# Kernel tuning notes

Measured on AMD Instinct MI355X. Metric: run time of the kernel, lower is better.

## Reference

```python
import jax, jax.numpy as jnp
import numpy as np

B, S, T = 32, 512, 128   # batch, source chars, target (protoform) chars
V, L = 128, 5            # char vocab len(C2I), number of languages
E, H, F = 512, 1024, 2048  # embedding_dim, model_size, feedforward_dim
START_CHAR, SEP_LANG = 1, L - 1


def setup_inputs() -> dict:
    key = jax.random.key(0)
    ks = jax.random.split(key, 32)
    f32 = jnp.float32

    def n(k, shape, fan_in):
        return jax.random.normal(k, shape, dtype=f32) * (1.0 / np.sqrt(fan_in))

    inp = {
        "src_chars": jax.random.randint(ks[0], (B, S), 0, V),
        "src_langs": jax.random.randint(ks[1], (B, S), 0, L),
        "tgt_chars": jax.random.randint(ks[2], (B, T), 0, V),
        # embedding feature extractor
        "char_emb": jax.random.normal(ks[3], (V, E), dtype=f32) * 0.02,
        "lang_emb": jax.random.normal(ks[4], (L, E), dtype=f32) * 0.02,
        "fc_W": n(ks[5], (E, 2 * E), 2 * E),
        "fc_b": jnp.zeros((E,), f32),
        # encoder GRU (PyTorch gate layout r,z,n)
        "enc_Wi": n(ks[6], (3 * H, E), E),
        "enc_Wh": n(ks[7], (3 * H, H), H),
        "enc_bi": jnp.zeros((3 * H,), f32),
        "enc_bh": jnp.zeros((3 * H,), f32),
        # decoder GRU, input = [E ; H]
        "dec_Wi": n(ks[8], (3 * H, E + H), E + H),
        "dec_Wh": n(ks[9], (3 * H, H), H),
        "dec_bi": jnp.zeros((3 * H,), f32),
        "dec_bh": jnp.zeros((3 * H,), f32),
        # attention
        "Wq": n(ks[10], (H, H), H),
        "Wk": n(ks[11], (H, H), H),
        "Wcs": n(ks[12], (H, E), E),
        # MLP H -> 2F -> F -> V
        "W1": n(ks[13], (2 * F, H), H),
        "b1": jnp.zeros((2 * F,), f32),
        "W2": n(ks[14], (F, 2 * F), 2 * F),
        "b2": jnp.zeros((F,), f32),
        "W3": n(ks[15], (V, F), F),
    }
    return inp


def _gru_step(h, x, Wi, Wh, bi, bh):
    gi = x @ Wi.T + bi            # [B, 3H]
    gh = h @ Wh.T + bh            # [B, 3H]
    ir, iz, inn = jnp.split(gi, 3, axis=-1)
    hr, hz, hn = jnp.split(gh, 3, axis=-1)
    r = jax.nn.sigmoid(ir + hr)
    z = jax.nn.sigmoid(iz + hz)
    n = jnp.tanh(inn + r * hn)
    return (1.0 - z) * n + z * h


def _mlp(x, W1, b1, W2, b2, W3):
    h = jax.nn.relu(x @ W1.T + b1)
    h = jax.nn.relu(h @ W2.T + b2)
    return h @ W3.T               # [B, V]


def reference(src_chars, src_langs, tgt_chars,
              char_emb, lang_emb, fc_W, fc_b,
              enc_Wi, enc_Wh, enc_bi, enc_bh,
              dec_Wi, dec_Wh, dec_bi, dec_bh,
              Wq, Wk, Wcs,
              W1, b1, W2, b2, W3):
    # --- feature extraction: concat(char_emb, lang_emb) -> Linear(2E -> E) ---
    def embed(c_idx, l_idx):
        ce = char_emb[c_idx]                       # [..., E]
        le = lang_emb[l_idx]                       # [..., E]
        return jnp.concatenate([ce, le], -1) @ fc_W.T + fc_b

    encoded = embed(src_chars, src_langs)          # [B, S, E]

    # --- encoder GRU over source chars ---
    def enc_step(h, x_t):
        h = _gru_step(h, x_t, enc_Wi, enc_Wh, enc_bi, enc_bh)
        return h, h

    h0 = jnp.zeros((encoded.shape[0], enc_Wh.shape[1]), encoded.dtype)
    _, enc_states = jax.lax.scan(enc_step, h0, jnp.swapaxes(encoded, 0, 1))
    enc_states = jnp.swapaxes(enc_states, 0, 1)    # [B, S, H]

    # precompute attention values: W_c_s(encoded) + W_key(keys)  [B, S, H]
    att_vals = encoded @ Wcs.T + enc_states @ Wk.T

    # --- initial decoder step: <s> embedding + last encoder state ---
    start_emb = embed(jnp.full((encoded.shape[0],), START_CHAR),
                      jnp.full((encoded.shape[0],), SEP_LANG))  # [B, E]
    context0 = enc_states[:, -1]                   # [B, H]
    d0 = jnp.zeros_like(context0)
    dec_h = _gru_step(d0, jnp.concatenate([start_emb, context0], -1),
                      dec_Wi, dec_Wh, dec_bi, dec_bh)

    tgt_emb = embed(tgt_chars, jnp.full_like(tgt_chars, SEP_LANG))  # [B, T, E]

    # --- decode T steps with teacher forcing ---
    def dec_step(carry, x_t):
        h, ctx = carry
        scores_t = _mlp(h + ctx, W1, b1, W2, b2, W3)           # [B, V]
        q = h @ Wq.T                                           # [B, H]
        att = jnp.einsum('bsh,bh->bs', enc_states, q)
        w = jax.nn.softmax(att, axis=-1)
        ctx_new = jnp.einsum('bs,bsh->bh', w, att_vals)        # [B, H]
        h_new = _gru_step(h, jnp.concatenate([x_t, ctx_new], -1),
                          dec_Wi, dec_Wh, dec_bi, dec_bh)
        return (h_new, ctx_new), scores_t

    (_, _), scores = jax.lax.scan(dec_step, (dec_h, context0),
                                  jnp.swapaxes(tgt_emb, 0, 1))
    return jnp.swapaxes(scores, 0, 1)              # [B, T, V]
```

## Files before the change

kernel.cpp:

```cpp
#include <hip/hip_runtime.h>
#include <math.h>


#define Bb 32
#define Ss 512
#define Tt 128
#define Vv 128
#define Hh 1024
#define H3 3072
#define APAD 40

typedef __attribute__((ext_vector_type(8))) short bf16x8;
typedef __attribute__((ext_vector_type(4))) float f32x4;

__device__ inline f32x4 mfma_bf16(bf16x8 a, bf16x8 b, f32x4 c) {
  return __builtin_amdgcn_mfma_f32_16x16x32_bf16(a, b, c, 0, 0, 0);
}
__device__ inline unsigned short f2bf(float f) {
  unsigned u = __builtin_bit_cast(unsigned, f);
  unsigned r = (u + 0x7fffu + ((u >> 16) & 1u)) >> 16;
  return (unsigned short)r;
}
__device__ inline float lof(unsigned u) { return __builtin_bit_cast(float, u << 16); }
__device__ inline float hif(unsigned u) { return __builtin_bit_cast(float, u & 0xffff0000u); }
__device__ inline float bf2f(unsigned short h) {
  return __builtin_bit_cast(float, ((unsigned)h) << 16);
}

#define O_ESBF   0UL
#define O_ESQ    33554432UL
#define O_AVBF   67108864UL
#define O_HCBF   100663296UL
#define O_WHE    109051904UL
#define O_WHD    115343360UL
#define O_WIC    121634816UL
#define O_WKB    127926272UL
#define O_WQT    130023424UL
#define O_W1B    132120576UL
#define O_W2B    140509184UL
#define O_W3B    157286400UL
#define O_XCAT   157810688UL
#define O_EMBFC  160432128UL
#define O_GITAB  161742848UL
#define O_AVTAB  169607168UL
#define O_DGIXT  172228608UL
#define O_GH     173801472UL
#define O_GI     174194688UL
#define O_H      174587904UL
#define O_HBF    174718976UL
#define O_CTX    174784512UL
#define O_CTXBF  174915584UL
#define O_ATTL   174981120UL

__global__ void k_xcat(const float* __restrict__ ce, const float* __restrict__ le,
                       float* __restrict__ xcat) {
  int row = blockIdx.x;
  int l = row >> 7, c = row & 127;
  int i = threadIdx.x * 4;
  float4 v;
  if (i < 512) v = *(const float4*)(ce + c * 512 + i);
  else         v = *(const float4*)(le + l * 512 + (i - 512));
  *(float4*)(xcat + (size_t)row * 1024 + i) = v;
}

__global__ void k_cltab(const int* __restrict__ sc, const int* __restrict__ sl,
                        int* __restrict__ cl) {
  int i = blockIdx.x * 256 + threadIdx.x;
  int b = i >> 9, s = i & 511;
  cl[s * 32 + b] = sl[b * Ss + s] * 128 + sc[b * Ss + s];
}

__global__ void k_cvt(const float* __restrict__ src, int ld, int lc,
                      unsigned short* __restrict__ dst) {
  size_t i = ((size_t)blockIdx.x * 256 + threadIdx.x) * 8;
  size_t r = i >> lc;
  int c = (int)(i & ((1u << lc) - 1));
  const float* s = src + r * (size_t)ld + c;
  float4 v0 = *(const float4*)s;
  float4 v1 = *(const float4*)(s + 4);
  union { unsigned short us[8]; uint4 u; } o;
  o.us[0] = f2bf(v0.x); o.us[1] = f2bf(v0.y); o.us[2] = f2bf(v0.z); o.us[3] = f2bf(v0.w);
  o.us[4] = f2bf(v1.x); o.us[5] = f2bf(v1.y); o.us[6] = f2bf(v1.z); o.us[7] = f2bf(v1.w);
  *(uint4*)(dst + i) = o.u;
}

__global__ void k_transcvt(const float* __restrict__ in, unsigned short* __restrict__ out) {
  __shared__ float t[32][33];
  int c0 = blockIdx.x * 32, r0 = blockIdx.y * 32;
  int tx = threadIdx.x, ty = threadIdx.y;
  for (int i = ty; i < 32; i += 8)
    t[i][tx] = in[(size_t)(r0 + i) * 1024 + c0 + tx];
  __syncthreads();
  for (int i = ty; i < 32; i += 8)
    out[(size_t)(c0 + i) * 1024 + r0 + tx] = f2bf(t[tx][i]);
}

template <bool BIAS>
__global__ __launch_bounds__(256) void k_gemm(
    const float* __restrict__ A, int lda, const float* __restrict__ W, int ldw,
    const float* __restrict__ bias, float* __restrict__ C, int ldc, int K) {
  __shared__ float As[8][128];
  __shared__ float Ws[8][128];
  int tid = threadIdx.x;
  int n0 = blockIdx.x * 128, m0 = blockIdx.y * 128;
  int tx = tid & 15, ty = tid >> 4;
  int lrow = tid >> 1, lseg = (tid & 1) * 4;
  const float* Ap = A + (size_t)(m0 + lrow) * lda + lseg;
  const float* Wp = W + (size_t)(n0 + lrow) * ldw + lseg;
  float acc[8][8];
#pragma unroll
  for (int i = 0; i < 8; ++i)
#pragma unroll
    for (int j = 0; j < 8; ++j) acc[i][j] = 0.f;
  for (int kt = 0; kt < K; kt += 8) {
    float4 av = *(const float4*)(Ap + kt);
    float4 wv = *(const float4*)(Wp + kt);
    __syncthreads();
    As[lseg + 0][lrow] = av.x; As[lseg + 1][lrow] = av.y;
    As[lseg + 2][lrow] = av.z; As[lseg + 3][lrow] = av.w;
    Ws[lseg + 0][lrow] = wv.x; Ws[lseg + 1][lrow] = wv.y;
    Ws[lseg + 2][lrow] = wv.z; Ws[lseg + 3][lrow] = wv.w;
    __syncthreads();
#pragma unroll
    for (int kk = 0; kk < 8; ++kk) {
      float a[8], b[8];
      *(float4*)(a + 0) = *(const float4*)(&As[kk][ty * 8 + 0]);
      *(float4*)(a + 4) = *(const float4*)(&As[kk][ty * 8 + 4]);
      *(float4*)(b + 0) = *(const float4*)(&Ws[kk][tx * 8 + 0]);
      *(float4*)(b + 4) = *(const float4*)(&Ws[kk][tx * 8 + 4]);
#pragma unroll
      for (int i = 0; i < 8; ++i)
#pragma unroll
        for (int j = 0; j < 8; ++j) acc[i][j] = fmaf(a[i], b[j], acc[i][j]);
    }
  }
#pragma unroll
  for (int i = 0; i < 8; ++i) {
    int r = m0 + ty * 8 + i;
#pragma unroll
    for (int j = 0; j < 8; ++j) {
      int c = n0 + tx * 8 + j;
      float v = acc[i][j];
      if (BIAS) v += bias[c];
      C[(size_t)r * ldc + c] = v;
    }
  }
}

template <int EPI, bool RELU, bool BIAS>
__global__ __launch_bounds__(256) void k_bgemm(
    const unsigned short* __restrict__ A, int lda,
    const unsigned short* __restrict__ W, int ldw,
    const float* __restrict__ bias, void* __restrict__ Cout, int ldc, int K,
    const float* __restrict__ avtab, const int* __restrict__ gl,
    const int* __restrict__ gc) {
  __shared__ unsigned short As[128 * APAD];
  __shared__ unsigned short Bs[128 * APAD];
  int tid = threadIdx.x;
  int n0 = blockIdx.x * 128, m0 = blockIdx.y * 128;
  int w = tid >> 6, l = tid & 63;
  int mw = (w & 1) * 64, nw = (w >> 1) * 64;
  int lrow = tid >> 1, lk = (tid & 1) * 16;
  const unsigned short* Ap = A + (size_t)(m0 + lrow) * lda + lk;
  const unsigned short* Wp = W + (size_t)(n0 + lrow) * ldw + lk;
  int fr = l & 15, fk = (l >> 4) * 8;
  f32x4 acc[4][4];
#pragma unroll
  for (int i = 0; i < 4; ++i)
#pragma unroll
    for (int j = 0; j < 4; ++j) acc[i][j] = (f32x4){0.f, 0.f, 0.f, 0.f};
  for (int kt = 0; kt < K; kt += 32) {
    uint4 a0 = *(const uint4*)(Ap + kt);
    uint4 a1 = *(const uint4*)(Ap + kt + 8);
    uint4 b0 = *(const uint4*)(Wp + kt);
    uint4 b1 = *(const uint4*)(Wp + kt + 8);
    __syncthreads();
    *(uint4*)&As[lrow * APAD + lk] = a0;
    *(uint4*)&As[lrow * APAD + lk + 8] = a1;
    *(uint4*)&Bs[lrow * APAD + lk] = b0;
    *(uint4*)&Bs[lrow * APAD + lk + 8] = b1;
    __syncthreads();
    bf16x8 af[4], bfg[4];
#pragma unroll
    for (int i = 0; i < 4; ++i) af[i] = *(const bf16x8*)&As[(mw + i * 16 + fr) * APAD + fk];
#pragma unroll
    for (int j = 0; j < 4; ++j) bfg[j] = *(const bf16x8*)&Bs[(nw + j * 16 + fr) * APAD + fk];
#pragma unroll
    for (int i = 0; i < 4; ++i)
#pragma unroll
      for (int j = 0; j < 4; ++j) acc[i][j] = mfma_bf16(af[i], bfg[j], acc[i][j]);
  }
#pragma unroll
  for (int i = 0; i < 4; ++i)
#pragma unroll
    for (int j = 0; j < 4; ++j) {
      int col = n0 + nw + j * 16 + fr;
#pragma unroll
      for (int r = 0; r < 4; ++r) {
        int row = m0 + mw + i * 16 + (l >> 4) * 4 + r;
        float v = acc[i][j][r];
        if (BIAS) v += bias[col];
        if (RELU) v = fmaxf(v, 0.f);
        if (EPI == 0) {
          ((unsigned short*)Cout)[(size_t)row * ldc + col] = f2bf(v);
        } else if (EPI == 1) {
          int cl = gl[row] * 128 + gc[row];
          ((unsigned short*)Cout)[(size_t)row * ldc + col] =
              f2bf(v + avtab[(size_t)cl * 1024 + col]);
        } else {
          int tt = row >> 5, bb = row & 31;
          ((float*)Cout)[(size_t)bb * (Tt * Vv) + tt * Vv + col] = v;
        }
      }
    }
}

template <int MODE>
__global__ __launch_bounds__(512) void k_step(
    const unsigned short* __restrict__ Wh,
    const unsigned short* __restrict__ Abf,
    const float* __restrict__ gtab,
    const int* __restrict__ idx,
    const float* __restrict__ ghb,
    const float* __restrict__ bh,
    float* __restrict__ h,
    unsigned short* __restrict__ hbfW,
    unsigned short* __restrict__ esb,
    int s, int flags) {
  __shared__ f32x4 red[8 * 6 * 64];
  int tid = threadIdx.x;
  int w = tid >> 6, l = tid & 63;
  int fr = l & 15, q = l >> 4;
  int j = blockIdx.x * 16 + fr;
  f32x4 acc[2][3];
#pragma unroll
  for (int m = 0; m < 2; ++m)
#pragma unroll
    for (int g = 0; g < 3; ++g) acc[m][g] = (f32x4){0.f, 0.f, 0.f, 0.f};
  if (!(flags & 4)) {
    int kb = w * 128 + q * 8;
    const unsigned short* A0 = Abf + fr * 1024 + kb;
    const unsigned short* W0 = Wh + (size_t)j * 1024 + kb;
#pragma unroll
    for (int kt = 0; kt < 128; kt += 32) {
      bf16x8 a0 = *(const bf16x8*)(A0 + kt);
      bf16x8 a1 = *(const bf16x8*)(A0 + 16 * 1024 + kt);
      bf16x8 b0 = *(const bf16x8*)(W0 + kt);
      bf16x8 b1 = *(const bf16x8*)(W0 + 1024 * 1024 + kt);
      bf16x8 b2 = *(const bf16x8*)(W0 + 2048 * 1024 + kt);
      acc[0][0] = mfma_bf16(a0, b0, acc[0][0]);
      acc[1][0] = mfma_bf16(a1, b0, acc[1][0]);
      acc[0][1] = mfma_bf16(a0, b1, acc[0][1]);
      acc[1][1] = mfma_bf16(a1, b1, acc[1][1]);
      acc[0][2] = mfma_bf16(a0, b2, acc[0][2]);
      acc[1][2] = mfma_bf16(a1, b2, acc[1][2]);
    }
  }
#pragma unroll
  for (int m = 0; m < 2; ++m)
#pragma unroll
    for (int g = 0; g < 3; ++g)
      red[(w * 6 + m * 3 + g) * 64 + l] = acc[m][g];
  __syncthreads();
  if (w >= 2) return;
  int m = w;
  f32x4 as_[3];
#pragma unroll
  for (int g = 0; g < 3; ++g) as_[g] = (f32x4){0.f, 0.f, 0.f, 0.f};
#pragma unroll
  for (int ww = 0; ww < 8; ++ww)
#pragma unroll
    for (int g = 0; g < 3; ++g)
      as_[g] = as_[g] + red[(ww * 6 + m * 3 + g) * 64 + l];
  float bhr = bh[j], bhz = bh[1024 + j], bhn = bh[2048 + j];
#pragma unroll
  for (int r = 0; r < 4; ++r) {
    int b = m * 16 + q * 4 + r;
    int c = (MODE == 0) ? idx[s * 32 + b] : ((flags & 2) ? 1 : idx[b * Tt + s]);
    const float* gp = gtab + (size_t)c * H3 + j;
    float gir = gp[0], giz = gp[1024], gin = gp[2048];
    float ghr = bhr, ghz = bhz, ghn = bhn;
    if (MODE == 0) {
      ghr += as_[0][r]; ghz += as_[1][r]; ghn += as_[2][r];
    } else {
      gir += as_[0][r]; giz += as_[1][r]; gin += as_[2][r];
      if (!(flags & 1)) {
        const float* g2 = ghb + b * H3 + j;
        ghr += g2[0]; ghz += g2[1024]; ghn += g2[2048];
      }
    }
    float rg = 1.f / (1.f + expf(-(gir + ghr)));
    float zg = 1.f / (1.f + expf(-(giz + ghz)));
    float ng = tanhf(gin + rg * ghn);
    float hold = (flags & 1) ? 0.f : h[b * 1024 + j];
    float hn = (1.f - zg) * ng + zg * hold;
    h[b * 1024 + j] = hn;
    unsigned short hb = f2bf(hn);
    hbfW[b * 1024 + j] = hb;
    if (MODE == 0) esb[((size_t)b * Ss + s) * 1024 + j] = hb;
  }
}

__global__ __launch_bounds__(256) void k_rec(
    const unsigned short* __restrict__ A, const unsigned short* __restrict__ W,
    float* __restrict__ C, int N, int nrec,
    const unsigned short* __restrict__ esq, const float* __restrict__ h,
    const float* __restrict__ ctx, float* __restrict__ attL,
    unsigned short* __restrict__ hc) {
  __shared__ unsigned short As[32 * 1024];
  int tid = threadIdx.x;
  int id = blockIdx.x;
  if (id < nrec) {
    {
      const uint4* src = (const uint4*)A;
      uint4* dst = (uint4*)As;
#pragma unroll
      for (int i = 0; i < 16; ++i) {
        int c = i * 256 + tid;
        int m = c >> 7, kc = c & 127;
        dst[m * 128 + (kc ^ (m & 7))] = src[c];
      }
    }
    __syncthreads();
    int w = tid >> 6, l = tid & 63;
    int nb = id * 64 + w * 16;
    int fr = l & 15, fk8 = (l >> 4);
    const unsigned short* Wp = W + (size_t)(nb + fr) * 1024 + fk8 * 8;
    const bf16x8* Asv = (const bf16x8*)As;
    f32x4 acc0 = (f32x4){0.f, 0.f, 0.f, 0.f}, acc1 = acc0;
#pragma unroll 8
    for (int kt = 0; kt < 1024; kt += 32) {
      int kc8 = (kt >> 3) + fk8;
      bf16x8 bw = *(const bf16x8*)(Wp + kt);
      bf16x8 a0 = Asv[fr * 128 + (kc8 ^ (fr & 7))];
      bf16x8 a1 = Asv[(fr + 16) * 128 + (kc8 ^ (fr & 7))];
      acc0 = mfma_bf16(a0, bw, acc0);
      acc1 = mfma_bf16(a1, bw, acc1);
    }
    int col = nb + fr;
    int rb = (l >> 4) * 4;
#pragma unroll
    for (int r = 0; r < 4; ++r) {
      C[(size_t)(rb + r) * N + col] = acc0[r];
      C[(size_t)(rb + r + 16) * N + col] = acc1[r];
    }
  } else {
    float* hs = (float*)As;
    int a = id - nrec, b = a >> 3, sc = a & 7;
    for (int i = tid; i < 1024; i += 256) hs[i] = h[b * 1024 + i];
    __syncthreads();
    if (sc < 4) {
      int j = sc * 256 + tid;
      hc[b * 1024 + j] = f2bf(hs[j] + ctx[b * 1024 + j]);
    }
    int sg = tid >> 2, li = tid & 3;
    int s = sc * 64 + sg;
    const unsigned short* ep = esq + (size_t)(b * 512 + s) * 1024;
    float acc = 0.f;
#pragma unroll 4
    for (int i = 0; i < 32; ++i) {
      int k = (i * 4 + li) * 8;
      uint4 e = *(const uint4*)(ep + k);
      float4 h0 = *(const float4*)&hs[k];
      float4 h1 = *(const float4*)&hs[k + 4];
      acc += lof(e.x) * h0.x + hif(e.x) * h0.y + lof(e.y) * h0.z + hif(e.y) * h0.w +
             lof(e.z) * h1.x + hif(e.z) * h1.y + lof(e.w) * h1.z + hif(e.w) * h1.w;
    }
    acc += __shfl_xor(acc, 1);
    acc += __shfl_xor(acc, 2);
    if (li == 0) attL[b * 512 + s] = acc;
  }
}

__global__ void k_ctxinit(const float* __restrict__ h, float* __restrict__ ctx,
                          unsigned short* __restrict__ ctxbf) {
  int idx = blockIdx.x * 256 + threadIdx.x;
  float v = h[idx];
  ctx[idx] = v;
  ctxbf[idx] = f2bf(v);
}

__global__ __launch_bounds__(256) void k_ctxsm(const float* __restrict__ attL,
                                               const unsigned short* __restrict__ av,
                                               float* __restrict__ ctx,
                                               unsigned short* __restrict__ ctxbf) {
  int jt = blockIdx.x, b = blockIdx.y;
  __shared__ float w[512];
  __shared__ float wm[4];
  __shared__ float wsm[4];
  __shared__ float red2[128];
  int tid = threadIdx.x;
  float a0 = attL[b * Ss + tid * 2];
  float a1 = attL[b * Ss + tid * 2 + 1];
  float m = fmaxf(a0, a1);
  for (int d = 1; d < 64; d <<= 1) m = fmaxf(m, __shfl_xor(m, d));
  if ((tid & 63) == 0) wm[tid >> 6] = m;
  __syncthreads();
  m = fmaxf(fmaxf(wm[0], wm[1]), fmaxf(wm[2], wm[3]));
  float e0 = expf(a0 - m), e1 = expf(a1 - m);
  w[tid * 2] = e0;
  w[tid * 2 + 1] = e1;
  float ssum = e0 + e1;
  for (int d = 1; d < 64; d <<= 1) ssum += __shfl_xor(ssum, d);
  if ((tid & 63) == 0) wsm[tid >> 6] = ssum;
  __syncthreads();
  float scale = 1.f / (wsm[0] + wsm[1] + wsm[2] + wsm[3]);
  int j = jt * 128 + (tid & 127);
  int sh = tid >> 7;
  const unsigned short* avp = av + (size_t)(b * Ss + sh * 256) * Hh + j;
  float acc = 0.f;
#pragma unroll 16
  for (int s = 0; s < 256; ++s) acc += w[sh * 256 + s] * bf2f(avp[(size_t)s * Hh]);
  if (sh == 1) red2[tid & 127] = acc;
  __syncthreads();
  if (sh == 0) {
    float v = (acc + red2[tid & 127]) * scale;
    ctx[b * Hh + j] = v;
    ctxbf[b * Hh + j] = f2bf(v);
  }
}

extern "C" void kernel_launch(void* const* d_in, const int* in_sizes, int n_in,
                              void* d_out, int out_size, void* d_ws, size_t ws_size,
                              hipStream_t stream) {
  (void)in_sizes; (void)n_in; (void)out_size; (void)ws_size;
  const int*   src_chars = (const int*)d_in[0];
  const int*   src_langs = (const int*)d_in[1];
  const int*   tgt_chars = (const int*)d_in[2];
  const float* char_emb  = (const float*)d_in[3];
  const float* lang_emb  = (const float*)d_in[4];
  const float* fc_W  = (const float*)d_in[5];
  const float* fc_b  = (const float*)d_in[6];
  const float* enc_Wi = (const float*)d_in[7];
  const float* enc_Wh = (const float*)d_in[8];
  const float* enc_bi = (const float*)d_in[9];
  const float* enc_bh = (const float*)d_in[10];
  const float* dec_Wi = (const float*)d_in[11];
  const float* dec_Wh = (const float*)d_in[12];
  const float* dec_bi = (const float*)d_in[13];
  const float* dec_bh = (const float*)d_in[14];
  const float* Wq  = (const float*)d_in[15];
  const float* Wk  = (const float*)d_in[16];
  const float* Wcs = (const float*)d_in[17];
  const float* W1 = (const float*)d_in[18];
  const float* b1 = (const float*)d_in[19];
  const float* W2 = (const float*)d_in[20];
  const float* b2 = (const float*)d_in[21];
  const float* W3 = (const float*)d_in[22];
  float* out = (float*)d_out;

  char* ws = (char*)d_ws;
  unsigned short* esbf  = (unsigned short*)(ws + O_ESBF);
  unsigned short* esq   = (unsigned short*)(ws + O_ESQ);
  unsigned short* avbf  = (unsigned short*)(ws + O_AVBF);
  unsigned short* hcbf  = (unsigned short*)(ws + O_HCBF);
  unsigned short* WheB  = (unsigned short*)(ws + O_WHE);
  unsigned short* WhdB  = (unsigned short*)(ws + O_WHD);
  unsigned short* WicB  = (unsigned short*)(ws + O_WIC);
  unsigned short* WkB   = (unsigned short*)(ws + O_WKB);
  unsigned short* WqTB  = (unsigned short*)(ws + O_WQT);
  unsigned short* W1B   = (unsigned short*)(ws + O_W1B);
  unsigned short* W2B   = (unsigned short*)(ws + O_W2B);
  unsigned short* W3B   = (unsigned short*)(ws + O_W3B);
  float* xcat   = (float*)(ws + O_XCAT);
  float* embfc  = (float*)(ws + O_EMBFC);
  float* gitab  = (float*)(ws + O_GITAB);
  float* avtab  = (float*)(ws + O_AVTAB);
  float* dgixt  = (float*)(ws + O_DGIXT);
  float* ghbuf  = (float*)(ws + O_GH);
  float* h      = (float*)(ws + O_H);
  unsigned short* hbf   = (unsigned short*)(ws + O_HBF);
  float* ctx    = (float*)(ws + O_CTX);
  unsigned short* ctxbf = (unsigned short*)(ws + O_CTXBF);
  float* attL   = (float*)(ws + O_ATTL);
  unsigned short* G1 = esq;
  unsigned short* G2 = avbf;
  int* cltab = (int*)(ws + O_GI);
  unsigned short* hbf2 = (unsigned short*)(ws + O_GI + 65536);

  dim3 blk(256);

  k_xcat<<<640, blk, 0, stream>>>(char_emb, lang_emb, xcat);
  k_cltab<<<64, blk, 0, stream>>>(src_chars, src_langs, cltab);
  k_gemm<true><<<dim3(4, 5), blk, 0, stream>>>(xcat, 1024, fc_W, 1024, fc_b, embfc, 512, 1024);
  k_gemm<true><<<dim3(24, 5), blk, 0, stream>>>(embfc, 512, enc_Wi, 512, enc_bi, gitab, H3, 512);
  k_gemm<false><<<dim3(8, 5), blk, 0, stream>>>(embfc, 512, Wcs, 512, nullptr, avtab, Hh, 512);
  k_gemm<true><<<dim3(24, 1), blk, 0, stream>>>(embfc + 512 * 512, 512, dec_Wi, 1536, dec_bi,
                                                dgixt, H3, 512);
  k_cvt<<<1536, blk, 0, stream>>>(enc_Wh, 1024, 10, WheB);
  k_cvt<<<1536, blk, 0, stream>>>(dec_Wh, 1024, 10, WhdB);
  k_cvt<<<1536, blk, 0, stream>>>(dec_Wi + 512, 1536, 10, WicB);
  k_cvt<<<512,  blk, 0, stream>>>(Wk, 1024, 10, WkB);
  k_cvt<<<2048, blk, 0, stream>>>(W1, 1024, 10, W1B);
  k_cvt<<<4096, blk, 0, stream>>>(W2, 4096, 12, W2B);
  k_cvt<<<128,  blk, 0, stream>>>(W3, 2048, 11, W3B);
  k_transcvt<<<dim3(32, 32), dim3(32, 8), 0, stream>>>(Wq, WqTB);

  for (int s = 0; s < Ss; ++s) {
    unsigned short* wb = (s & 1) ? hbf2 : hbf;
    const unsigned short* rb = (s & 1) ? hbf : hbf2;
    k_step<0><<<64, 512, 0, stream>>>(WheB, rb, gitab, cltab, nullptr, enc_bh,
                                      h, wb, esbf, s, s == 0 ? 5 : 0);
  }

  k_bgemm<0, false, false><<<dim3(8, 128), blk, 0, stream>>>(
      esbf, 1024, WqTB, 1024, nullptr, esq, 1024, 1024, nullptr, nullptr, nullptr);
  k_bgemm<1, false, false><<<dim3(8, 128), blk, 0, stream>>>(
      esbf, 1024, WkB, 1024, nullptr, avbf, 1024, 1024, avtab, src_langs, src_chars);

  k_ctxinit<<<128, blk, 0, stream>>>(h, ctx, ctxbf);
  k_step<1><<<64, 512, 0, stream>>>(WicB, ctxbf, dgixt, tgt_chars, nullptr, dec_bh,
                                    h, hbf, nullptr, 0, 3);

  for (int t = 0; t < Tt; ++t) {
    k_rec<<<304, blk, 0, stream>>>(hbf, WhdB, ghbuf, H3, 48,
                                   esq, h, ctx, attL, hcbf + (size_t)t * Bb * Hh);
    if (t == Tt - 1) break;
    k_ctxsm<<<dim3(8, 32), blk, 0, stream>>>(attL, avbf, ctx, ctxbf);
    k_step<1><<<64, 512, 0, stream>>>(WicB, ctxbf, dgixt, tgt_chars, ghbuf, dec_bh,
                                      h, hbf, nullptr, t, 0);
  }

  k_bgemm<0, true, true><<<dim3(32, 32), blk, 0, stream>>>(
      hcbf, 1024, W1B, 1024, b1, G1, 4096, 1024, nullptr, nullptr, nullptr);
  k_bgemm<0, true, true><<<dim3(16, 32), blk, 0, stream>>>(
      G1, 4096, W2B, 4096, b2, G2, 2048, 4096, nullptr, nullptr, nullptr);
  k_bgemm<2, false, false><<<dim3(1, 32), blk, 0, stream>>>(
      G2, 2048, W3B, 2048, nullptr, out, 0, 2048, nullptr, nullptr, nullptr);
}
```

Measured before the change: 9.784 ms.

## Replace per-step encoder GRU launches with persistent cooperative kernel and grid barrier

The 512 per-timestep encoder GRU kernel launches become one cooperative persistent kernel of 64 blocks. Each block keeps its slice of the recurrent weights (96 KB, XOR-swizzled) resident in shared memory and holds its hidden state in registers. Timesteps are synchronised with an atomic-counter grid barrier that is reset in k_cltab. This removes launch overhead and the repeated weight reloads from global memory, at the cost of the barrier spin latency each step and a dependence on all 64 blocks being co-resident.

```diff
diff --git a/kernel.cpp b/kernel.cpp
--- a/kernel.cpp
+++ b/kernel.cpp
@@ -9,6 +9,7 @@
 #define Hh 1024
 #define H3 3072
 #define APAD 40
+#define NBE 64
 
 typedef __attribute__((ext_vector_type(8))) short bf16x8;
 typedef __attribute__((ext_vector_type(4))) float f32x4;
@@ -64,7 +65,8 @@
 }
 
 __global__ void k_cltab(const int* __restrict__ sc, const int* __restrict__ sl,
-                        int* __restrict__ cl) {
+                        int* __restrict__ cl, int* __restrict__ bar) {
+  if (blockIdx.x == 0 && threadIdx.x == 0) *bar = 0;
   int i = blockIdx.x * 256 + threadIdx.x;
   int b = i >> 9, s = i & 511;
   cl[s * 32 + b] = sl[b * Ss + s] * 128 + sc[b * Ss + s];
@@ -213,6 +215,112 @@
         }
       }
     }
+}
+
+__global__ __launch_bounds__(512) void k_enc_pers(
+    const unsigned short* __restrict__ Whe, const float* __restrict__ gitab,
+    const int* __restrict__ cltab, const float* __restrict__ bh,
+    float* __restrict__ h, unsigned short* __restrict__ hbf0,
+    unsigned short* __restrict__ hbf1, unsigned short* __restrict__ esb,
+    int* __restrict__ bar) {
+  __shared__ unsigned short Ws[48 * 1024];
+  __shared__ f32x4 red[8 * 6 * 64];
+  int tid = threadIdx.x;
+  int blk = blockIdx.x;
+  int w = tid >> 6, l = tid & 63;
+  int fr = l & 15, q = l >> 4;
+  int j = blk * 16 + fr;
+  {
+    uint4* dst = (uint4*)Ws;
+    const uint4* src = (const uint4*)Whe;
+#pragma unroll
+    for (int it = 0; it < 12; ++it) {
+      int idx = it * 512 + tid;
+      int lr = idx >> 7, c = idx & 127;
+      int grow = (lr >> 4) * 1024 + blk * 16 + (lr & 15);
+      dst[lr * 128 + (c ^ (lr & 7))] = src[(size_t)grow * 128 + c];
+    }
+  }
+  float bhr = bh[j], bhz = bh[1024 + j], bhn = bh[2048 + j];
+  float hold[4] = {0.f, 0.f, 0.f, 0.f};
+  __syncthreads();
+  const bf16x8* Wsv = (const bf16x8*)Ws;
+  for (int s = 0; s < Ss; ++s) {
+    unsigned short* wb = (s & 1) ? hbf1 : hbf0;
+    const unsigned short* rb = (s & 1) ? hbf0 : hbf1;
+    float gi0[4], gi1[4], gi2[4];
+    if (w < 2) {
+#pragma unroll
+      for (int r = 0; r < 4; ++r) {
+        int b = w * 16 + q * 4 + r;
+        int c = cltab[s * 32 + b];
+        const float* gp = gitab + (size_t)c * H3 + j;
+        gi0[r] = gp[0]; gi1[r] = gp[1024]; gi2[r] = gp[2048];
+      }
+    }
+    f32x4 acc[2][3];
+#pragma unroll
+    for (int m = 0; m < 2; ++m)
+#pragma unroll
+      for (int g = 0; g < 3; ++g) acc[m][g] = (f32x4){0.f, 0.f, 0.f, 0.f};
+    if (s > 0) {
+      int kb = w * 128 + q * 8;
+      const unsigned short* A0 = rb + fr * 1024 + kb;
+#pragma unroll
+      for (int kt = 0; kt < 128; kt += 32) {
+        bf16x8 a0 = *(const bf16x8*)(A0 + kt);
+        bf16x8 a1 = *(const bf16x8*)(A0 + 16 * 1024 + kt);
+        int c8 = (kb + kt) >> 3;
+#pragma unroll
+        for (int g = 0; g < 3; ++g) {
+          bf16x8 bw = Wsv[(g * 16 + fr) * 128 + (c8 ^ (fr & 7))];
+          acc[0][g] = mfma_bf16(a0, bw, acc[0][g]);
+          acc[1][g] = mfma_bf16(a1, bw, acc[1][g]);
+        }
+      }
+    }
+#pragma unroll
+    for (int m = 0; m < 2; ++m)
+#pragma unroll
+      for (int g = 0; g < 3; ++g)
+        red[(w * 6 + m * 3 + g) * 64 + l] = acc[m][g];
+    __syncthreads();
+    if (w < 2) {
+      int m = w;
+      f32x4 as_[3];
+#pragma unroll
+      for (int g = 0; g < 3; ++g) as_[g] = (f32x4){0.f, 0.f, 0.f, 0.f};
+#pragma unroll
+      for (int ww = 0; ww < 8; ++ww)
+#pragma unroll
+        for (int g = 0; g < 3; ++g)
+          as_[g] = as_[g] + red[(ww * 6 + m * 3 + g) * 64 + l];
+#pragma unroll
+      for (int r = 0; r < 4; ++r) {
+        int b = m * 16 + q * 4 + r;
+        float ghr = bhr, ghz = bhz, ghn = bhn;
+        ghr += as_[0][r]; ghz += as_[1][r]; ghn += as_[2][r];
+        float rg = 1.f / (1.f + expf(-(gi0[r] + ghr)));
+        float zg = 1.f / (1.f + expf(-(gi1[r] + ghz)));
+        float ng = tanhf(gi2[r] + rg * ghn);
+        float hn = (1.f - zg) * ng + zg * hold[r];
+        hold[r] = hn;
+        unsigned short hb = f2bf(hn);
+        wb[b * 1024 + j] = hb;
+        esb[((size_t)b * Ss + s) * 1024 + j] = hb;
+        if (s == Ss - 1) h[b * 1024 + j] = hn;
+      }
+    }
+    __syncthreads();
+    if (tid == 0) {
+      __hip_atomic_fetch_add(bar, 1, __ATOMIC_RELEASE, __HIP_MEMORY_SCOPE_AGENT);
+      int tgt = NBE * (s + 1);
+      while (__hip_atomic_load(bar, __ATOMIC_RELAXED, __HIP_MEMORY_SCOPE_AGENT) < tgt)
+        __builtin_amdgcn_s_sleep(1);
+      __builtin_amdgcn_fence(__ATOMIC_ACQUIRE, "agent");
+    }
+    __syncthreads();
+  }
 }
 
 template <int MODE>
@@ -477,11 +585,12 @@
   unsigned short* G2 = avbf;
   int* cltab = (int*)(ws + O_GI);
   unsigned short* hbf2 = (unsigned short*)(ws + O_GI + 65536);
+  int* bar = (int*)(ws + O_GI + 131072);
 
   dim3 blk(256);
 
   k_xcat<<<640, blk, 0, stream>>>(char_emb, lang_emb, xcat);
-  k_cltab<<<64, blk, 0, stream>>>(src_chars, src_langs, cltab);
+  k_cltab<<<64, blk, 0, stream>>>(src_chars, src_langs, cltab, bar);
   k_gemm<true><<<dim3(4, 5), blk, 0, stream>>>(xcat, 1024, fc_W, 1024, fc_b, embfc, 512, 1024);
   k_gemm<true><<<dim3(24, 5), blk, 0, stream>>>(embfc, 512, enc_Wi, 512, enc_bi, gitab, H3, 512);
   k_gemm<false><<<dim3(8, 5), blk, 0, stream>>>(embfc, 512, Wcs, 512, nullptr, avtab, Hh, 512);
@@ -496,11 +605,20 @@
   k_cvt<<<128,  blk, 0, stream>>>(W3, 2048, 11, W3B);
   k_transcvt<<<dim3(32, 32), dim3(32, 8), 0, stream>>>(Wq, WqTB);
 
-  for (int s = 0; s < Ss; ++s) {
-    unsigned short* wb = (s & 1) ? hbf2 : hbf;
-    const unsigned short* rb = (s & 1) ? hbf : hbf2;
-    k_step<0><<<64, 512, 0, stream>>>(WheB, rb, gitab, cltab, nullptr, enc_bh,
-                                      h, wb, esbf, s, s == 0 ? 5 : 0);
+  {
+    const unsigned short* p_whe = WheB;
+    const float* p_git = gitab;
+    const int* p_cl = cltab;
+    const float* p_bh = enc_bh;
+    float* p_h = h;
+    unsigned short* p_h0 = hbf;
+    unsigned short* p_h1 = hbf2;
+    unsigned short* p_esb = esbf;
+    int* p_bar = bar;
+    void* kargs[] = {(void*)&p_whe, (void*)&p_git, (void*)&p_cl, (void*)&p_bh,
+                     (void*)&p_h, (void*)&p_h0, (void*)&p_h1, (void*)&p_esb,
+                     (void*)&p_bar};
+    hipLaunchCooperativeKernel((const void*)k_enc_pers, dim3(NBE), dim3(512), kargs, 0, stream);
   }
 
   k_bgemm<0, false, false><<<dim3(8, 128), blk, 0, stream>>>(
```

Result: faster. 8.790 ms (-10.2%).
